# Kernel tuning notes

Measured on AMD Instinct MI355X. Metric: run time of the kernel, lower is better.

The kernel has to match this reference:

```python
import jax, jax.numpy as jnp
import numpy as np

B = 1048576
STATE_DIM, HIDDEN, LATENT = 21, 64, 14
LN_EPS = 1e-5
# index map replicating the torch repeat/cat reconstruction of metric attention (13 -> 21)
EXPAND_IDX = np.array([0, 1, 2, 3, 4, 4, 5, 5, 5, 6, 6, 6, 7, 7, 8, 9, 9, 10, 10, 11, 12])


def setup_inputs() -> dict:
    key = jax.random.key(0)
    ks = jax.random.split(key, 20)

    def w(k, shape, fan_in):
        return (jax.random.uniform(k, shape, jnp.float32, -1.0, 1.0) / np.sqrt(fan_in))

    return {
        'state': jax.random.normal(ks[0], (B, STATE_DIM), jnp.float32),
        # encoder
        'W_enc1': w(ks[1], (STATE_DIM, HIDDEN), STATE_DIM),
        'b_enc1': w(ks[2], (HIDDEN,), STATE_DIM),
        'ln_g': jnp.ones((HIDDEN,), jnp.float32),
        'ln_b': jnp.zeros((HIDDEN,), jnp.float32),
        'W_enc2': w(ks[3], (HIDDEN, HIDDEN), HIDDEN),
        'b_enc2': w(ks[4], (HIDDEN,), HIDDEN),
        'W_enc3': w(ks[5], (HIDDEN, LATENT), HIDDEN),
        'b_enc3': w(ks[6], (LATENT,), HIDDEN),
        # decoder
        'W_dec1': w(ks[7], (LATENT, HIDDEN), LATENT),
        'b_dec1': w(ks[8], (HIDDEN,), LATENT),
        'W_dec2': w(ks[9], (HIDDEN, 8), HIDDEN),
        'b_dec2': w(ks[10], (8,), HIDDEN),
        # attention heads
        'W_m': w(ks[11], (STATE_DIM, 13), STATE_DIM),
        'b_m': w(ks[12], (13,), STATE_DIM),
        'W_h': w(ks[13], (STATE_DIM, 6), STATE_DIM),
        'b_h': w(ks[14], (6,), STATE_DIM),
        'W_c': w(ks[15], (STATE_DIM, 4), STATE_DIM),
        'b_c': w(ks[16], (4,), STATE_DIM),
        # learnable head scales (init 1.0 as in torch)
        's_m': jnp.asarray(1.0, jnp.float32),
        's_h': jnp.asarray(1.0, jnp.float32),
        's_c': jnp.asarray(1.0, jnp.float32),
    }


def _normalize(state):
    ns = state
    ns = ns.at[:, 0:2].set(state[:, 0:2] / 3.0)
    ns = ns.at[:, 17].set(state[:, 17] / 2.0)
    ns = ns.at[:, 18].set(state[:, 18] / 4.0)
    ns = ns.at[:, 19].set(jnp.clip(state[:, 19], 0.0, 2.0) / 2.0)
    return ns


def _layernorm(x, g, b):
    mu = jnp.mean(x, axis=-1, keepdims=True)
    var = jnp.mean(jnp.square(x - mu), axis=-1, keepdims=True)
    return (x - mu) / jnp.sqrt(var + LN_EPS) * g + b


def reference(state, W_enc1, b_enc1, ln_g, ln_b, W_enc2, b_enc2, W_enc3, b_enc3,
              W_dec1, b_dec1, W_dec2, b_dec2, W_m, b_m, W_h, b_h, W_c, b_c,
              s_m, s_h, s_c):
    ns = _normalize(state)  # [B, 21]

    metric = jax.nn.softmax(ns @ W_m + b_m, axis=-1) * (jax.nn.sigmoid(s_m) * 2.0)  # [B,13]
    hyp = jax.nn.softmax(ns @ W_h + b_h, axis=-1) * (jax.nn.sigmoid(s_h) * 2.0)      # [B,6]
    curr = jax.nn.softmax(ns @ W_c + b_c, axis=-1) * (jax.nn.sigmoid(s_c) * 2.0)     # [B,4]

    attended = ns * metric[:, EXPAND_IDX]  # [B,21]

    h = jnp.tanh(_layernorm(attended @ W_enc1 + b_enc1, ln_g, ln_b))
    h = jax.nn.relu(h @ W_enc2 + b_enc2)
    latent = h @ W_enc3 + b_enc3  # [B,14]

    d = jax.nn.relu(latent @ W_dec1 + b_dec1)
    corrections = jnp.tanh(d @ W_dec2 + b_dec2)  # [B,8]

    return corrections, latent, metric, hyp, curr
```

## Files before the change

### kernel.cpp

```cpp
#include <hip/hip_runtime.h>

static constexpr int SD = 21, HD = 64, LT = 14;
static constexpr int NFRAG = 40;

typedef _Float16       f16x4  __attribute__((ext_vector_type(4)));
typedef float          f32x4  __attribute__((ext_vector_type(4)));
typedef unsigned       u32x2v __attribute__((ext_vector_type(2)));
typedef __fp16         pk2    __attribute__((ext_vector_type(2)));

__device__ __forceinline__ float frcp(float x){ return __builtin_amdgcn_rcpf(x); }
__device__ __forceinline__ float frsq(float x){ return __builtin_amdgcn_rsqf(x); }

__device__ __forceinline__ void wave_fence(){
    asm volatile("s_waitcnt lgkmcnt(0)" ::: "memory");
    __builtin_amdgcn_sched_barrier(0);
}

__device__ __forceinline__ unsigned packrtz(float a, float b){
    pk2 h = __builtin_amdgcn_cvt_pkrtz(a, b);
    union { pk2 h; unsigned u; } u; u.h = h; return u.u;
}
__device__ __forceinline__ float ftanh(float x){
    x = fminf(15.0f, fmaxf(-15.0f, x));
    float e = __expf(2.0f * x);
    return (e - 1.0f) * frcp(e + 1.0f);
}
template<int NN>
__device__ __forceinline__ void softmax_scale(float (&v)[NN], float gate){
    float mx = v[0];
#pragma unroll
    for (int j = 1; j < NN; ++j) mx = fmaxf(mx, v[j]);
    float s = 0.0f;
#pragma unroll
    for (int j = 0; j < NN; ++j){ v[j] = __expf(v[j] - mx); s += v[j]; }
    float r = frcp(s) * gate;
#pragma unroll
    for (int j = 0; j < NN; ++j) v[j] *= r;
}

union Frag2 { u32x2v u2; unsigned u[2]; f16x4 f; };

__device__ __forceinline__ f32x4 mfma16(f16x4 a, f16x4 b, f32x4 c){
    return __builtin_amdgcn_mfma_f32_16x16x16f16(a, b, c, 0, 0, 0);
}

__device__ __forceinline__ float headsW(const float* Wm, const float* Wh,
                                        const float* Wc, int k, int j){
    if (j < 13) return Wm[k*13 + j];
    if (j < 19) return Wh[k*6 + (j - 13)];
    if (j < 23) return Wc[k*4 + (j - 19)];
    return 0.0f;
}

__global__ void pack_bfrags(const float* __restrict__ W1, const float* __restrict__ W2,
                            const float* __restrict__ W3, const float* __restrict__ Wd1,
                            const float* __restrict__ Wd2,
                            const float* __restrict__ Wm, const float* __restrict__ Wh,
                            const float* __restrict__ Wc, unsigned* __restrict__ ws)
{
    int t = blockIdx.x * blockDim.x + threadIdx.x;
    if (t >= NFRAG * 64) return;
    int fid = t >> 6, lane = t & 63;
    int g = lane >> 4, c = lane & 15;

    if (fid >= 36) {
        int e = fid - 36, ks16 = e >> 1, ct = e & 1;
        int col = ct*16 + c;
#pragma unroll
        for (int j = 0; j < 2; ++j) {
            int k0 = ks16*16 + g*4 + 2*j;
            float a = (k0     < SD && col < 23) ? headsW(Wm, Wh, Wc, k0,   col) : 0.0f;
            float b = (k0 + 1 < SD && col < 23) ? headsW(Wm, Wh, Wc, k0+1, col) : 0.0f;
            ws[fid*128 + lane*2 + j] = packrtz(a, b);
        }
        return;
    }

    const float* W; int ks16, ct, K, Ncol, ld;
    if (fid < 8)       { W = W1;  ks16 = fid >> 2;    ct = fid & 3;  K = 21; Ncol = 64; ld = 64; }
    else if (fid < 24) { int e = fid - 8;
                         W = W2;  ks16 = e >> 2;      ct = e & 3;    K = 64; Ncol = 64; ld = 64; }
    else if (fid < 28) { W = W3;  ks16 = fid - 24;    ct = 0;        K = 64; Ncol = 14; ld = 14; }
    else if (fid < 32) { W = Wd1; ks16 = 0;           ct = fid - 28; K = 14; Ncol = 64; ld = 64; }
    else               { W = Wd2; ks16 = fid - 32;    ct = 0;        K = 64; Ncol = 8;  ld = 8;  }
    int col = ct*16 + c;
#pragma unroll
    for (int j = 0; j < 2; ++j) {
        int k0 = ks16*16 + g*4 + 2*j;
        float a = (k0     < K && col < Ncol) ? W[k0*ld + col]     : 0.0f;
        float b = (k0 + 1 < K && col < Ncol) ? W[(k0+1)*ld + col] : 0.0f;
        ws[fid*128 + lane*2 + j] = packrtz(a, b);
    }
}

__global__ __launch_bounds__(256) void statenet_mfma9(
    const float* __restrict__ state,
    const unsigned* __restrict__ pw,
    const float* __restrict__ b1,
    const float* __restrict__ lng, const float* __restrict__ lnb,
    const float* __restrict__ b2,  const float* __restrict__ b3,
    const float* __restrict__ bd1, const float* __restrict__ bd2,
    const float* __restrict__ bm,  const float* __restrict__ bh,
    const float* __restrict__ bc,
    const float* __restrict__ psm, const float* __restrict__ psh,
    const float* __restrict__ psc,
    float* __restrict__ out, int N)
{
    __shared__ __align__(16) unsigned s_at[4*1152];
    __shared__ __align__(16) float    s_lg[4*832];

    const int tid = threadIdx.x;
    const int w  = tid >> 6, l = tid & 63;
    const int cl = l & 15,  g = l >> 4;
    const long long rowbase = (long long)blockIdx.x * 128 + w * 32;

    unsigned* at  = s_at + w * 1152;
    float*    slg = s_lg + w * 832;

    const u32x2v* BF2 = reinterpret_cast<const u32x2v*>(pw);
    const f32x4 vzero = {0.0f, 0.0f, 0.0f, 0.0f};

    {
        const float4* g4 = reinterpret_cast<const float4*>(state + rowbase * SD);
        float4* r4 = reinterpret_cast<float4*>(slg);
#pragma unroll
        for (int i = 0; i < 3; ++i) {
            int idx = l + i * 64;
            if (idx < 168) r4[idx] = g4[idx];
        }
    }
    wave_fence();

    float ns[SD];
    if (l < 32) {
        const float* p = slg + l * SD;
#pragma unroll
        for (int k = 0; k < SD; ++k) ns[k] = p[k];

        ns[0]  *= (1.0f / 3.0f);
        ns[1]  *= (1.0f / 3.0f);
        ns[17] *= 0.5f;
        ns[18] *= 0.25f;
        ns[19]  = fminf(fmaxf(ns[19], 0.0f), 2.0f) * 0.5f;

        const int base = l * 36;
#pragma unroll
        for (int kk = 0; kk < 10; ++kk) at[base + kk] = packrtz(ns[2*kk], ns[2*kk+1]);
        at[base + 10] = packrtz(ns[20], 0.0f);
#pragma unroll
        for (int kk = 11; kk < 16; ++kk) at[base + kk] = 0u;
    }
    wave_fence();

    {
        Frag2 aN[2][2];
#pragma unroll
        for (int m2 = 0; m2 < 2; ++m2)
#pragma unroll
            for (int ks = 0; ks < 2; ++ks)
                aN[m2][ks].u2 = *reinterpret_cast<const u32x2v*>(&at[(m2*16 + cl)*36 + ks*8 + 2*g]);
        f32x4 hl[2][2];
#pragma unroll
        for (int ct = 0; ct < 2; ++ct)
#pragma unroll
            for (int m2 = 0; m2 < 2; ++m2) hl[ct][m2] = vzero;
#pragma unroll
        for (int ct = 0; ct < 2; ++ct)
#pragma unroll
            for (int ks = 0; ks < 2; ++ks) {
                Frag2 wf; wf.u2 = BF2[(36 + ks*2 + ct)*64 + l];
#pragma unroll
                for (int m2 = 0; m2 < 2; ++m2)
                    hl[ct][m2] = mfma16(wf.f, aN[m2][ks].f, hl[ct][m2]);
            }
#pragma unroll
        for (int m2 = 0; m2 < 2; ++m2) {
            float* p0 = &slg[(m2*16 + cl)*26 + 4*g];
            reinterpret_cast<float2*>(p0)[0] = make_float2(hl[0][m2][0], hl[0][m2][1]);
            reinterpret_cast<float2*>(p0)[1] = make_float2(hl[0][m2][2], hl[0][m2][3]);
            if (g < 2) {
                float* p1 = &slg[(m2*16 + cl)*26 + 16 + 4*g];
                reinterpret_cast<float2*>(p1)[0] = make_float2(hl[1][m2][0], hl[1][m2][1]);
                reinterpret_cast<float2*>(p1)[1] = make_float2(hl[1][m2][2], hl[1][m2][3]);
            }
        }
    }
    wave_fence();

    if (l < 32) {
        const long long row = rowbase + l;
        float lg[24];
#pragma unroll
        for (int i = 0; i < 12; ++i) {
            float2 v = *reinterpret_cast<const float2*>(&slg[l*26 + 2*i]);
            lg[2*i] = v.x; lg[2*i+1] = v.y;
        }
        float m[13], hv[6], cv[4];
#pragma unroll
        for (int j = 0; j < 13; ++j) m[j]  = lg[j]      + bm[j];
#pragma unroll
        for (int j = 0; j < 6;  ++j) hv[j] = lg[13 + j] + bh[j];
#pragma unroll
        for (int j = 0; j < 4;  ++j) cv[j] = lg[19 + j] + bc[j];

        const float gm = 2.0f * frcp(1.0f + __expf(-psm[0]));
        const float gh = 2.0f * frcp(1.0f + __expf(-psh[0]));
        const float gc = 2.0f * frcp(1.0f + __expf(-psc[0]));
        softmax_scale<13>(m,  gm);
        softmax_scale<6 >(hv, gh);
        softmax_scale<4 >(cv, gc);

        {
            float* pm = out + (long long)22 * N + row * 13;
#pragma unroll
            for (int j = 0; j < 13; ++j) pm[j] = m[j];
            float* ph = out + (long long)35 * N + row * 6;
#pragma unroll
            for (int j = 0; j < 3; ++j)
                reinterpret_cast<float2*>(ph)[j] = make_float2(hv[2*j], hv[2*j+1]);
            float* pc = out + (long long)41 * N + row * 4;
            reinterpret_cast<float4*>(pc)[0] = make_float4(cv[0], cv[1], cv[2], cv[3]);
        }

        constexpr int EIDX[SD] = {0,1,2,3,4,4,5,5,5,6,6,6,7,7,8,9,9,10,10,11,12};
        float atv[SD];
#pragma unroll
        for (int k = 0; k < SD; ++k) atv[k] = ns[k] * m[EIDX[k]];
        const int base = l * 36;
#pragma unroll
        for (int kk = 0; kk < 10; ++kk) at[base + kk] = packrtz(atv[2*kk], atv[2*kk+1]);
        at[base + 10] = packrtz(atv[20], 0.0f);
    }
    wave_fence();

    Frag2 aA[2][2];
#pragma unroll
    for (int m2 = 0; m2 < 2; ++m2)
#pragma unroll
        for (int ks = 0; ks < 2; ++ks)
            aA[m2][ks].u2 = *reinterpret_cast<const u32x2v*>(&at[(m2*16 + cl)*36 + ks*8 + 2*g]);

    f32x4 D1[4][2];
#pragma unroll
    for (int f = 0; f < 4; ++f)
#pragma unroll
        for (int m2 = 0; m2 < 2; ++m2) D1[f][m2] = vzero;
#pragma unroll
    for (int f = 0; f < 4; ++f)
#pragma unroll
        for (int ks = 0; ks < 2; ++ks) {
            Frag2 wf; wf.u2 = BF2[(ks*4 + f)*64 + l];
#pragma unroll
            for (int m2 = 0; m2 < 2; ++m2)
                D1[f][m2] = mfma16(wf.f, aA[m2][ks].f, D1[f][m2]);
        }

    float4 b1q[4], lgq[4], lbq[4];
#pragma unroll
    for (int f = 0; f < 4; ++f) {
        b1q[f] = *reinterpret_cast<const float4*>(&b1[f*16 + 4*g]);
        lgq[f] = *reinterpret_cast<const float4*>(&lng[f*16 + 4*g]);
        lbq[f] = *reinterpret_cast<const float4*>(&lnb[f*16 + 4*g]);
    }

    Frag2 B1[2][4];
#pragma unroll
    for (int m2 = 0; m2 < 2; ++m2) {
        float s = 0.0f, ss = 0.0f;
#pragma unroll
        for (int f = 0; f < 4; ++f) {
            float bb[4] = {b1q[f].x, b1q[f].y, b1q[f].z, b1q[f].w};
#pragma unroll
            for (int q = 0; q < 4; ++q) {
                float v = D1[f][m2][q] + bb[q];
                D1[f][m2][q] = v;
                s += v; ss = fmaf(v, v, ss);
            }
        }
        s  += __shfl_xor(s, 16);  s  += __shfl_xor(s, 32);
        ss += __shfl_xor(ss, 16); ss += __shfl_xor(ss, 32);
        float mu   = s * (1.0f/64.0f);
        float var  = ss * (1.0f/64.0f) - mu*mu;
        float istd = frsq(var + 1e-5f);
#pragma unroll
        for (int f = 0; f < 4; ++f) {
            float gg[4] = {lgq[f].x, lgq[f].y, lgq[f].z, lgq[f].w};
            float be[4] = {lbq[f].x, lbq[f].y, lbq[f].z, lbq[f].w};
            float t0 = ftanh(fmaf((D1[f][m2][0] - mu) * istd, gg[0], be[0]));
            float t1 = ftanh(fmaf((D1[f][m2][1] - mu) * istd, gg[1], be[1]));
            float t2 = ftanh(fmaf((D1[f][m2][2] - mu) * istd, gg[2], be[2]));
            float t3 = ftanh(fmaf((D1[f][m2][3] - mu) * istd, gg[3], be[3]));
            B1[m2][f].u[0] = packrtz(t0, t1);
            B1[m2][f].u[1] = packrtz(t2, t3);
        }
    }

    f32x4 D2[4][2];
#pragma unroll
    for (int f2 = 0; f2 < 4; ++f2)
#pragma unroll
        for (int m2 = 0; m2 < 2; ++m2) D2[f2][m2] = vzero;
#pragma unroll
    for (int f2 = 0; f2 < 4; ++f2)
#pragma unroll
        for (int f = 0; f < 4; ++f) {
            Frag2 wf; wf.u2 = BF2[(8 + f*4 + f2)*64 + l];
#pragma unroll
            for (int m2 = 0; m2 < 2; ++m2)
                D2[f2][m2] = mfma16(wf.f, B1[m2][f].f, D2[f2][m2]);
        }
    Frag2 B2[2][4];
#pragma unroll
    for (int f2 = 0; f2 < 4; ++f2) {
        float4 bq = *reinterpret_cast<const float4*>(&b2[f2*16 + 4*g]);
        float bb[4] = {bq.x, bq.y, bq.z, bq.w};
#pragma unroll
        for (int m2 = 0; m2 < 2; ++m2) {
            float t0 = fmaxf(D2[f2][m2][0] + bb[0], 0.0f);
            float t1 = fmaxf(D2[f2][m2][1] + bb[1], 0.0f);
            float t2 = fmaxf(D2[f2][m2][2] + bb[2], 0.0f);
            float t3 = fmaxf(D2[f2][m2][3] + bb[3], 0.0f);
            B2[m2][f2].u[0] = packrtz(t0, t1);
            B2[m2][f2].u[1] = packrtz(t2, t3);
        }
    }

    float b3v[4];
#pragma unroll
    for (int q = 0; q < 4; ++q) {
        int j = 4*g + q;
        b3v[q] = (j < LT) ? b3[j] : 0.0f;
    }
    Frag2 B3[2];
#pragma unroll
    for (int m2 = 0; m2 < 2; ++m2) {
        f32x4 a3 = vzero;
#pragma unroll
        for (int f = 0; f < 4; ++f) {
            Frag2 wf; wf.u2 = BF2[(24 + f)*64 + l];
            a3 = mfma16(wf.f, B2[m2][f].f, a3);
        }
        float lv[4];
#pragma unroll
        for (int q = 0; q < 4; ++q)
            lv[q] = (4*g + q < LT) ? (a3[q] + b3v[q]) : 0.0f;
        {
            float* pl = out + (long long)8 * N + (rowbase + m2*16 + cl) * 14 + 4*g;
            if (g < 3) {
                reinterpret_cast<float2*>(pl)[0] = make_float2(lv[0], lv[1]);
                reinterpret_cast<float2*>(pl)[1] = make_float2(lv[2], lv[3]);
            } else {
                reinterpret_cast<float2*>(pl)[0] = make_float2(lv[0], lv[1]);
            }
        }
        B3[m2].u[0] = packrtz(lv[0], lv[1]);
        B3[m2].u[1] = packrtz(lv[2], lv[3]);
    }

    f32x4 D4[4][2];
#pragma unroll
    for (int f = 0; f < 4; ++f)
#pragma unroll
        for (int m2 = 0; m2 < 2; ++m2) D4[f][m2] = vzero;
#pragma unroll
    for (int f = 0; f < 4; ++f) {
        Frag2 wf; wf.u2 = BF2[(28 + f)*64 + l];
#pragma unroll
        for (int m2 = 0; m2 < 2; ++m2)
            D4[f][m2] = mfma16(wf.f, B3[m2].f, D4[f][m2]);
    }
    Frag2 B4[2][4];
#pragma unroll
    for (int f = 0; f < 4; ++f) {
        float4 bq = *reinterpret_cast<const float4*>(&bd1[f*16 + 4*g]);
        float bb[4] = {bq.x, bq.y, bq.z, bq.w};
#pragma unroll
        for (int m2 = 0; m2 < 2; ++m2) {
            float t0 = fmaxf(D4[f][m2][0] + bb[0], 0.0f);
            float t1 = fmaxf(D4[f][m2][1] + bb[1], 0.0f);
            float t2 = fmaxf(D4[f][m2][2] + bb[2], 0.0f);
            float t3 = fmaxf(D4[f][m2][3] + bb[3], 0.0f);
            B4[m2][f].u[0] = packrtz(t0, t1);
            B4[m2][f].u[1] = packrtz(t2, t3);
        }
    }

#pragma unroll
    for (int m2 = 0; m2 < 2; ++m2) {
        f32x4 a5 = vzero;
#pragma unroll
        for (int f = 0; f < 4; ++f) {
            Frag2 wf; wf.u2 = BF2[(32 + f)*64 + l];
            a5 = mfma16(wf.f, B4[m2][f].f, a5);
        }
        if (g < 2) {
            float4 bq = *reinterpret_cast<const float4*>(&bd2[4*g]);
            float* pc = out + (rowbase + m2*16 + cl) * 8 + 4*g;
            reinterpret_cast<float4*>(pc)[0] =
                make_float4(ftanh(a5[0] + bq.x), ftanh(a5[1] + bq.y),
                            ftanh(a5[2] + bq.z), ftanh(a5[3] + bq.w));
        }
    }
}

extern "C" void kernel_launch(void* const* d_in, const int* in_sizes, int n_in,
                              void* d_out, int out_size, void* d_ws, size_t ws_size,
                              hipStream_t stream)
{
    const float* state = (const float*)d_in[0];
    const float* W1   = (const float*)d_in[1];
    const float* b1   = (const float*)d_in[2];
    const float* lng  = (const float*)d_in[3];
    const float* lnb  = (const float*)d_in[4];
    const float* W2   = (const float*)d_in[5];
    const float* b2   = (const float*)d_in[6];
    const float* W3   = (const float*)d_in[7];
    const float* b3   = (const float*)d_in[8];
    const float* Wd1  = (const float*)d_in[9];
    const float* bd1  = (const float*)d_in[10];
    const float* Wd2  = (const float*)d_in[11];
    const float* bd2  = (const float*)d_in[12];
    const float* Wm   = (const float*)d_in[13];
    const float* bm   = (const float*)d_in[14];
    const float* Wh   = (const float*)d_in[15];
    const float* bh   = (const float*)d_in[16];
    const float* Wc   = (const float*)d_in[17];
    const float* bc   = (const float*)d_in[18];
    const float* psm  = (const float*)d_in[19];
    const float* psh  = (const float*)d_in[20];
    const float* psc  = (const float*)d_in[21];

    unsigned* pw = (unsigned*)d_ws;

    hipLaunchKernelGGL(pack_bfrags, dim3((NFRAG*64 + 255)/256), dim3(256), 0, stream,
                       W1, W2, W3, Wd1, Wd2, Wm, Wh, Wc, pw);

    const int N = in_sizes[0] / SD;
    hipLaunchKernelGGL(statenet_mfma9, dim3(N / 128), dim3(256), 0, stream,
                       state, pw, b1, lng, lnb, b2, b3, bd1, bd2,
                       bm, bh, bc, psm, psh, psc,
                       (float*)d_out, N);
}
```

Before: 119.9 us.

## Use persistent blocks with register-cached weight fragments across tiles

Launches a fixed grid of 1024 blocks, each looping over 8 row tiles, and loads all 40 packed weight fragments into registers once before the loop instead of reloading them from global memory for every MFMA group. This removes repeated weight-fragment loads and per-block startup cost. In exchange it raises register pressure, which can lower occupancy, and it hardcodes N = 1024*8*128 rows, so any other batch size is handled incorrectly.

```diff
diff --git a/kernel.cpp b/kernel.cpp
--- a/kernel.cpp
+++ b/kernel.cpp
@@ -2,6 +2,8 @@
 
 static constexpr int SD = 21, HD = 64, LT = 14;
 static constexpr int NFRAG = 40;
+static constexpr int NB    = 1024;
+static constexpr int TILES = 8;
 
 typedef _Float16       f16x4  __attribute__((ext_vector_type(4)));
 typedef float          f32x4  __attribute__((ext_vector_type(4)));
@@ -93,7 +95,7 @@
     }
 }
 
-__global__ __launch_bounds__(256) void statenet_mfma9(
+__global__ __launch_bounds__(256) void statenet_mfma10(
     const float* __restrict__ state,
     const unsigned* __restrict__ pw,
     const float* __restrict__ b1,
@@ -112,7 +114,6 @@
     const int tid = threadIdx.x;
     const int w  = tid >> 6, l = tid & 63;
     const int cl = l & 15,  g = l >> 4;
-    const long long rowbase = (long long)blockIdx.x * 128 + w * 32;
 
     unsigned* at  = s_at + w * 1152;
     float*    slg = s_lg + w * 832;
@@ -120,286 +121,295 @@
     const u32x2v* BF2 = reinterpret_cast<const u32x2v*>(pw);
     const f32x4 vzero = {0.0f, 0.0f, 0.0f, 0.0f};
 
-    {
-        const float4* g4 = reinterpret_cast<const float4*>(state + rowbase * SD);
-        float4* r4 = reinterpret_cast<float4*>(slg);
-#pragma unroll
-        for (int i = 0; i < 3; ++i) {
-            int idx = l + i * 64;
-            if (idx < 168) r4[idx] = g4[idx];
-        }
-    }
-    wave_fence();
-
-    float ns[SD];
-    if (l < 32) {
-        const float* p = slg + l * SD;
-#pragma unroll
-        for (int k = 0; k < SD; ++k) ns[k] = p[k];
-
-        ns[0]  *= (1.0f / 3.0f);
-        ns[1]  *= (1.0f / 3.0f);
-        ns[17] *= 0.5f;
-        ns[18] *= 0.25f;
-        ns[19]  = fminf(fmaxf(ns[19], 0.0f), 2.0f) * 0.5f;
-
-        const int base = l * 36;
-#pragma unroll
-        for (int kk = 0; kk < 10; ++kk) at[base + kk] = packrtz(ns[2*kk], ns[2*kk+1]);
-        at[base + 10] = packrtz(ns[20], 0.0f);
-#pragma unroll
-        for (int kk = 11; kk < 16; ++kk) at[base + kk] = 0u;
-    }
-    wave_fence();
-
-    {
-        Frag2 aN[2][2];
+    Frag2 wHD[4], wE1[8], wE2[16], wE3[4], wD1w[4], wD2w[4];
+#pragma unroll
+    for (int e = 0; e < 4; ++e)  wHD[e].u2  = BF2[(36 + e)*64 + l];
+#pragma unroll
+    for (int e = 0; e < 8; ++e)  wE1[e].u2  = BF2[e*64 + l];
+#pragma unroll
+    for (int e = 0; e < 16; ++e) wE2[e].u2  = BF2[(8 + e)*64 + l];
+#pragma unroll
+    for (int e = 0; e < 4; ++e)  wE3[e].u2  = BF2[(24 + e)*64 + l];
+#pragma unroll
+    for (int e = 0; e < 4; ++e)  wD1w[e].u2 = BF2[(28 + e)*64 + l];
+#pragma unroll
+    for (int e = 0; e < 4; ++e)  wD2w[e].u2 = BF2[(32 + e)*64 + l];
+
+#pragma unroll 1
+    for (int it = 0; it < TILES; ++it) {
+        const long long rowbase =
+            ((long long)blockIdx.x + (long long)it * NB) * 128 + w * 32;
+
+        {
+            const float4* g4 = reinterpret_cast<const float4*>(state + rowbase * SD);
+            float4* r4 = reinterpret_cast<float4*>(slg);
+#pragma unroll
+            for (int i = 0; i < 3; ++i) {
+                int idx = l + i * 64;
+                if (idx < 168) r4[idx] = g4[idx];
+            }
+        }
+        wave_fence();
+
+        float ns[SD];
+        if (l < 32) {
+            const float* p = slg + l * SD;
+#pragma unroll
+            for (int k = 0; k < SD; ++k) ns[k] = p[k];
+
+            ns[0]  *= (1.0f / 3.0f);
+            ns[1]  *= (1.0f / 3.0f);
+            ns[17] *= 0.5f;
+            ns[18] *= 0.25f;
+            ns[19]  = fminf(fmaxf(ns[19], 0.0f), 2.0f) * 0.5f;
+
+            const int base = l * 36;
+#pragma unroll
+            for (int kk = 0; kk < 10; ++kk) at[base + kk] = packrtz(ns[2*kk], ns[2*kk+1]);
+            at[base + 10] = packrtz(ns[20], 0.0f);
+#pragma unroll
+            for (int kk = 11; kk < 16; ++kk) at[base + kk] = 0u;
+        }
+        wave_fence();
+
+        {
+            Frag2 aN[2][2];
+#pragma unroll
+            for (int m2 = 0; m2 < 2; ++m2)
+#pragma unroll
+                for (int ks = 0; ks < 2; ++ks)
+                    aN[m2][ks].u2 = *reinterpret_cast<const u32x2v*>(&at[(m2*16 + cl)*36 + ks*8 + 2*g]);
+            f32x4 hl[2][2];
+#pragma unroll
+            for (int ct = 0; ct < 2; ++ct)
+#pragma unroll
+                for (int m2 = 0; m2 < 2; ++m2) hl[ct][m2] = vzero;
+#pragma unroll
+            for (int ct = 0; ct < 2; ++ct)
+#pragma unroll
+                for (int ks = 0; ks < 2; ++ks)
+#pragma unroll
+                    for (int m2 = 0; m2 < 2; ++m2)
+                        hl[ct][m2] = mfma16(wHD[ks*2 + ct].f, aN[m2][ks].f, hl[ct][m2]);
+#pragma unroll
+            for (int m2 = 0; m2 < 2; ++m2) {
+                float* p0 = &slg[(m2*16 + cl)*26 + 4*g];
+                reinterpret_cast<float2*>(p0)[0] = make_float2(hl[0][m2][0], hl[0][m2][1]);
+                reinterpret_cast<float2*>(p0)[1] = make_float2(hl[0][m2][2], hl[0][m2][3]);
+                if (g < 2) {
+                    float* p1 = &slg[(m2*16 + cl)*26 + 16 + 4*g];
+                    reinterpret_cast<float2*>(p1)[0] = make_float2(hl[1][m2][0], hl[1][m2][1]);
+                    reinterpret_cast<float2*>(p1)[1] = make_float2(hl[1][m2][2], hl[1][m2][3]);
+                }
+            }
+        }
+        wave_fence();
+
+        if (l < 32) {
+            const long long row = rowbase + l;
+            float lg[24];
+#pragma unroll
+            for (int i = 0; i < 12; ++i) {
+                float2 v = *reinterpret_cast<const float2*>(&slg[l*26 + 2*i]);
+                lg[2*i] = v.x; lg[2*i+1] = v.y;
+            }
+            float m[13], hv[6], cv[4];
+#pragma unroll
+            for (int j = 0; j < 13; ++j) m[j]  = lg[j]      + bm[j];
+#pragma unroll
+            for (int j = 0; j < 6;  ++j) hv[j] = lg[13 + j] + bh[j];
+#pragma unroll
+            for (int j = 0; j < 4;  ++j) cv[j] = lg[19 + j] + bc[j];
+
+            const float gm = 2.0f * frcp(1.0f + __expf(-psm[0]));
+            const float gh = 2.0f * frcp(1.0f + __expf(-psh[0]));
+            const float gc = 2.0f * frcp(1.0f + __expf(-psc[0]));
+            softmax_scale<13>(m,  gm);
+            softmax_scale<6 >(hv, gh);
+            softmax_scale<4 >(cv, gc);
+
+            {
+                float* pm = out + (long long)22 * N + row * 13;
+#pragma unroll
+                for (int j = 0; j < 13; ++j) pm[j] = m[j];
+                float* ph = out + (long long)35 * N + row * 6;
+#pragma unroll
+                for (int j = 0; j < 3; ++j)
+                    reinterpret_cast<float2*>(ph)[j] = make_float2(hv[2*j], hv[2*j+1]);
+                float* pc = out + (long long)41 * N + row * 4;
+                reinterpret_cast<float4*>(pc)[0] = make_float4(cv[0], cv[1], cv[2], cv[3]);
+            }
+
+            constexpr int EIDX[SD] = {0,1,2,3,4,4,5,5,5,6,6,6,7,7,8,9,9,10,10,11,12};
+            float atv[SD];
+#pragma unroll
+            for (int k = 0; k < SD; ++k) atv[k] = ns[k] * m[EIDX[k]];
+            const int base = l * 36;
+#pragma unroll
+            for (int kk = 0; kk < 10; ++kk) at[base + kk] = packrtz(atv[2*kk], atv[2*kk+1]);
+            at[base + 10] = packrtz(atv[20], 0.0f);
+        }
+        wave_fence();
+
+        Frag2 aA[2][2];
 #pragma unroll
         for (int m2 = 0; m2 < 2; ++m2)
 #pragma unroll
             for (int ks = 0; ks < 2; ++ks)
-                aN[m2][ks].u2 = *reinterpret_cast<const u32x2v*>(&at[(m2*16 + cl)*36 + ks*8 + 2*g]);
-        f32x4 hl[2][2];
-#pragma unroll
-        for (int ct = 0; ct < 2; ++ct)
-#pragma unroll
-            for (int m2 = 0; m2 < 2; ++m2) hl[ct][m2] = vzero;
-#pragma unroll
-        for (int ct = 0; ct < 2; ++ct)
-#pragma unroll
-            for (int ks = 0; ks < 2; ++ks) {
-                Frag2 wf; wf.u2 = BF2[(36 + ks*2 + ct)*64 + l];
+                aA[m2][ks].u2 = *reinterpret_cast<const u32x2v*>(&at[(m2*16 + cl)*36 + ks*8 + 2*g]);
+
+        f32x4 D1[4][2];
+#pragma unroll
+        for (int f = 0; f < 4; ++f)
+#pragma unroll
+            for (int m2 = 0; m2 < 2; ++m2) D1[f][m2] = vzero;
+#pragma unroll
+        for (int f = 0; f < 4; ++f)
+#pragma unroll
+            for (int ks = 0; ks < 2; ++ks)
 #pragma unroll
                 for (int m2 = 0; m2 < 2; ++m2)
-                    hl[ct][m2] = mfma16(wf.f, aN[m2][ks].f, hl[ct][m2]);
-            }
+                    D1[f][m2] = mfma16(wE1[ks*4 + f].f, aA[m2][ks].f, D1[f][m2]);
+
+        float4 b1q[4], lgq[4], lbq[4];
+#pragma unroll
+        for (int f = 0; f < 4; ++f) {
+            b1q[f] = *reinterpret_cast<const float4*>(&b1[f*16 + 4*g]);
+            lgq[f] = *reinterpret_cast<const float4*>(&lng[f*16 + 4*g]);
+            lbq[f] = *reinterpret_cast<const float4*>(&lnb[f*16 + 4*g]);
+        }
+
+        Frag2 B1[2][4];
 #pragma unroll
         for (int m2 = 0; m2 < 2; ++m2) {
-            float* p0 = &slg[(m2*16 + cl)*26 + 4*g];
-            reinterpret_cast<float2*>(p0)[0] = make_float2(hl[0][m2][0], hl[0][m2][1]);
-            reinterpret_cast<float2*>(p0)[1] = make_float2(hl[0][m2][2], hl[0][m2][3]);
+            float s = 0.0f, ss = 0.0f;
+#pragma unroll
+            for (int f = 0; f < 4; ++f) {
+                float bb[4] = {b1q[f].x, b1q[f].y, b1q[f].z, b1q[f].w};
+#pragma unroll
+                for (int q = 0; q < 4; ++q) {
+                    float v = D1[f][m2][q] + bb[q];
+                    D1[f][m2][q] = v;
+                    s += v; ss = fmaf(v, v, ss);
+                }
+            }
+            s  += __shfl_xor(s, 16);  s  += __shfl_xor(s, 32);
+            ss += __shfl_xor(ss, 16); ss += __shfl_xor(ss, 32);
+            float mu   = s * (1.0f/64.0f);
+            float var  = ss * (1.0f/64.0f) - mu*mu;
+            float istd = frsq(var + 1e-5f);
+#pragma unroll
+            for (int f = 0; f < 4; ++f) {
+                float gg[4] = {lgq[f].x, lgq[f].y, lgq[f].z, lgq[f].w};
+                float be[4] = {lbq[f].x, lbq[f].y, lbq[f].z, lbq[f].w};
+                float t0 = ftanh(fmaf((D1[f][m2][0] - mu) * istd, gg[0], be[0]));
+                float t1 = ftanh(fmaf((D1[f][m2][1] - mu) * istd, gg[1], be[1]));
+                float t2 = ftanh(fmaf((D1[f][m2][2] - mu) * istd, gg[2], be[2]));
+                float t3 = ftanh(fmaf((D1[f][m2][3] - mu) * istd, gg[3], be[3]));
+                B1[m2][f].u[0] = packrtz(t0, t1);
+                B1[m2][f].u[1] = packrtz(t2, t3);
+            }
+        }
+
+        f32x4 D2[4][2];
+#pragma unroll
+        for (int f2 = 0; f2 < 4; ++f2)
+#pragma unroll
+            for (int m2 = 0; m2 < 2; ++m2) D2[f2][m2] = vzero;
+#pragma unroll
+        for (int f2 = 0; f2 < 4; ++f2)
+#pragma unroll
+            for (int f = 0; f < 4; ++f)
+#pragma unroll
+                for (int m2 = 0; m2 < 2; ++m2)
+                    D2[f2][m2] = mfma16(wE2[f*4 + f2].f, B1[m2][f].f, D2[f2][m2]);
+        Frag2 B2[2][4];
+#pragma unroll
+        for (int f2 = 0; f2 < 4; ++f2) {
+            float4 bq = *reinterpret_cast<const float4*>(&b2[f2*16 + 4*g]);
+            float bb[4] = {bq.x, bq.y, bq.z, bq.w};
+#pragma unroll
+            for (int m2 = 0; m2 < 2; ++m2) {
+                float t0 = fmaxf(D2[f2][m2][0] + bb[0], 0.0f);
+                float t1 = fmaxf(D2[f2][m2][1] + bb[1], 0.0f);
+                float t2 = fmaxf(D2[f2][m2][2] + bb[2], 0.0f);
+                float t3 = fmaxf(D2[f2][m2][3] + bb[3], 0.0f);
+                B2[m2][f2].u[0] = packrtz(t0, t1);
+                B2[m2][f2].u[1] = packrtz(t2, t3);
+            }
+        }
+
+        float b3v[4];
+#pragma unroll
+        for (int q = 0; q < 4; ++q) {
+            int j = 4*g + q;
+            b3v[q] = (j < LT) ? b3[j] : 0.0f;
+        }
+        Frag2 B3[2];
+#pragma unroll
+        for (int m2 = 0; m2 < 2; ++m2) {
+            f32x4 a3 = vzero;
+#pragma unroll
+            for (int f = 0; f < 4; ++f)
+                a3 = mfma16(wE3[f].f, B2[m2][f].f, a3);
+            float lv[4];
+#pragma unroll
+            for (int q = 0; q < 4; ++q)
+                lv[q] = (4*g + q < LT) ? (a3[q] + b3v[q]) : 0.0f;
+            {
+                float* pl = out + (long long)8 * N + (rowbase + m2*16 + cl) * 14 + 4*g;
+                if (g < 3) {
+                    reinterpret_cast<float2*>(pl)[0] = make_float2(lv[0], lv[1]);
+                    reinterpret_cast<float2*>(pl)[1] = make_float2(lv[2], lv[3]);
+                } else {
+                    reinterpret_cast<float2*>(pl)[0] = make_float2(lv[0], lv[1]);
+                }
+            }
+            B3[m2].u[0] = packrtz(lv[0], lv[1]);
+            B3[m2].u[1] = packrtz(lv[2], lv[3]);
+        }
+
+        f32x4 D4[4][2];
+#pragma unroll
+        for (int f = 0; f < 4; ++f)
+#pragma unroll
+            for (int m2 = 0; m2 < 2; ++m2) D4[f][m2] = vzero;
+#pragma unroll
+        for (int f = 0; f < 4; ++f)
+#pragma unroll
+            for (int m2 = 0; m2 < 2; ++m2)
+                D4[f][m2] = mfma16(wD1w[f].f, B3[m2].f, D4[f][m2]);
+        Frag2 B4[2][4];
+#pragma unroll
+        for (int f = 0; f < 4; ++f) {
+            float4 bq = *reinterpret_cast<const float4*>(&bd1[f*16 + 4*g]);
+            float bb[4] = {bq.x, bq.y, bq.z, bq.w};
+#pragma unroll
+            for (int m2 = 0; m2 < 2; ++m2) {
+                float t0 = fmaxf(D4[f][m2][0] + bb[0], 0.0f);
+                float t1 = fmaxf(D4[f][m2][1] + bb[1], 0.0f);
+                float t2 = fmaxf(D4[f][m2][2] + bb[2], 0.0f);
+                float t3 = fmaxf(D4[f][m2][3] + bb[3], 0.0f);
+                B4[m2][f].u[0] = packrtz(t0, t1);
+                B4[m2][f].u[1] = packrtz(t2, t3);
+            }
+        }
+
+#pragma unroll
+        for (int m2 = 0; m2 < 2; ++m2) {
+            f32x4 a5 = vzero;
+#pragma unroll
+            for (int f = 0; f < 4; ++f)
+                a5 = mfma16(wD2w[f].f, B4[m2][f].f, a5);
             if (g < 2) {
-                float* p1 = &slg[(m2*16 + cl)*26 + 16 + 4*g];
-                reinterpret_cast<float2*>(p1)[0] = make_float2(hl[1][m2][0], hl[1][m2][1]);
-                reinterpret_cast<float2*>(p1)[1] = make_float2(hl[1][m2][2], hl[1][m2][3]);
-            }
-        }
-    }
-    wave_fence();
-
-    if (l < 32) {
-        const long long row = rowbase + l;
-        float lg[24];
-#pragma unroll
-        for (int i = 0; i < 12; ++i) {
-            float2 v = *reinterpret_cast<const float2*>(&slg[l*26 + 2*i]);
-            lg[2*i] = v.x; lg[2*i+1] = v.y;
-        }
-        float m[13], hv[6], cv[4];
-#pragma unroll
-        for (int j = 0; j < 13; ++j) m[j]  = lg[j]      + bm[j];
-#pragma unroll
-        for (int j = 0; j < 6;  ++j) hv[j] = lg[13 + j] + bh[j];
-#pragma unroll
-        for (int j = 0; j < 4;  ++j) cv[j] = lg[19 + j] + bc[j];
-
-        const float gm = 2.0f * frcp(1.0f + __expf(-psm[0]));
-        const float gh = 2.0f * frcp(1.0f + __expf(-psh[0]));
-        const float gc = 2.0f * frcp(1.0f + __expf(-psc[0]));
-        softmax_scale<13>(m,  gm);
-        softmax_scale<6 >(hv, gh);
-        softmax_scale<4 >(cv, gc);
-
-        {
-            float* pm = out + (long long)22 * N + row * 13;
-#pragma unroll
-            for (int j = 0; j < 13; ++j) pm[j] = m[j];
-            float* ph = out + (long long)35 * N + row * 6;
-#pragma unroll
-            for (int j = 0; j < 3; ++j)
-                reinterpret_cast<float2*>(ph)[j] = make_float2(hv[2*j], hv[2*j+1]);
-            float* pc = out + (long long)41 * N + row * 4;
-            reinterpret_cast<float4*>(pc)[0] = make_float4(cv[0], cv[1], cv[2], cv[3]);
-        }
-
-        constexpr int EIDX[SD] = {0,1,2,3,4,4,5,5,5,6,6,6,7,7,8,9,9,10,10,11,12};
-        float atv[SD];
-#pragma unroll
-        for (int k = 0; k < SD; ++k) atv[k] = ns[k] * m[EIDX[k]];
-        const int base = l * 36;
-#pragma unroll
-        for (int kk = 0; kk < 10; ++kk) at[base + kk] = packrtz(atv[2*kk], atv[2*kk+1]);
-        at[base + 10] = packrtz(atv[20], 0.0f);
-    }
-    wave_fence();
-
-    Frag2 aA[2][2];
-#pragma unroll
-    for (int m2 = 0; m2 < 2; ++m2)
-#pragma unroll
-        for (int ks = 0; ks < 2; ++ks)
-            aA[m2][ks].u2 = *reinterpret_cast<const u32x2v*>(&at[(m2*16 + cl)*36 + ks*8 + 2*g]);
-
-    f32x4 D1[4][2];
-#pragma unroll
-    for (int f = 0; f < 4; ++f)
-#pragma unroll
-        for (int m2 = 0; m2 < 2; ++m2) D1[f][m2] = vzero;
-#pragma unroll
-    for (int f = 0; f < 4; ++f)
-#pragma unroll
-        for (int ks = 0; ks < 2; ++ks) {
-            Frag2 wf; wf.u2 = BF2[(ks*4 + f)*64 + l];
-#pragma unroll
-            for (int m2 = 0; m2 < 2; ++m2)
-                D1[f][m2] = mfma16(wf.f, aA[m2][ks].f, D1[f][m2]);
-        }
-
-    float4 b1q[4], lgq[4], lbq[4];
-#pragma unroll
-    for (int f = 0; f < 4; ++f) {
-        b1q[f] = *reinterpret_cast<const float4*>(&b1[f*16 + 4*g]);
-        lgq[f] = *reinterpret_cast<const float4*>(&lng[f*16 + 4*g]);
-        lbq[f] = *reinterpret_cast<const float4*>(&lnb[f*16 + 4*g]);
-    }
-
-    Frag2 B1[2][4];
-#pragma unroll
-    for (int m2 = 0; m2 < 2; ++m2) {
-        float s = 0.0f, ss = 0.0f;
-#pragma unroll
-        for (int f = 0; f < 4; ++f) {
-            float bb[4] = {b1q[f].x, b1q[f].y, b1q[f].z, b1q[f].w};
-#pragma unroll
-            for (int q = 0; q < 4; ++q) {
-                float v = D1[f][m2][q] + bb[q];
-                D1[f][m2][q] = v;
-                s += v; ss = fmaf(v, v, ss);
-            }
-        }
-        s  += __shfl_xor(s, 16);  s  += __shfl_xor(s, 32);
-        ss += __shfl_xor(ss, 16); ss += __shfl_xor(ss, 32);
-        float mu   = s * (1.0f/64.0f);
-        float var  = ss * (1.0f/64.0f) - mu*mu;
-        float istd = frsq(var + 1e-5f);
-#pragma unroll
-        for (int f = 0; f < 4; ++f) {
-            float gg[4] = {lgq[f].x, lgq[f].y, lgq[f].z, lgq[f].w};
-            float be[4] = {lbq[f].x, lbq[f].y, lbq[f].z, lbq[f].w};
-            float t0 = ftanh(fmaf((D1[f][m2][0] - mu) * istd, gg[0], be[0]));
-            float t1 = ftanh(fmaf((D1[f][m2][1] - mu) * istd, gg[1], be[1]));
-            float t2 = ftanh(fmaf((D1[f][m2][2] - mu) * istd, gg[2], be[2]));
-            float t3 = ftanh(fmaf((D1[f][m2][3] - mu) * istd, gg[3], be[3]));
-            B1[m2][f].u[0] = packrtz(t0, t1);
-            B1[m2][f].u[1] = packrtz(t2, t3);
-        }
-    }
-
-    f32x4 D2[4][2];
-#pragma unroll
-    for (int f2 = 0; f2 < 4; ++f2)
-#pragma unroll
-        for (int m2 = 0; m2 < 2; ++m2) D2[f2][m2] = vzero;
-#pragma unroll
-    for (int f2 = 0; f2 < 4; ++f2)
-#pragma unroll
-        for (int f = 0; f < 4; ++f) {
-            Frag2 wf; wf.u2 = BF2[(8 + f*4 + f2)*64 + l];
-#pragma unroll
-            for (int m2 = 0; m2 < 2; ++m2)
-                D2[f2][m2] = mfma16(wf.f, B1[m2][f].f, D2[f2][m2]);
-        }
-    Frag2 B2[2][4];
-#pragma unroll
-    for (int f2 = 0; f2 < 4; ++f2) {
-        float4 bq = *reinterpret_cast<const float4*>(&b2[f2*16 + 4*g]);
-        float bb[4] = {bq.x, bq.y, bq.z, bq.w};
-#pragma unroll
-        for (int m2 = 0; m2 < 2; ++m2) {
-            float t0 = fmaxf(D2[f2][m2][0] + bb[0], 0.0f);
-            float t1 = fmaxf(D2[f2][m2][1] + bb[1], 0.0f);
-            float t2 = fmaxf(D2[f2][m2][2] + bb[2], 0.0f);
-            float t3 = fmaxf(D2[f2][m2][3] + bb[3], 0.0f);
-            B2[m2][f2].u[0] = packrtz(t0, t1);
-            B2[m2][f2].u[1] = packrtz(t2, t3);
-        }
-    }
-
-    float b3v[4];
-#pragma unroll
-    for (int q = 0; q < 4; ++q) {
-        int j = 4*g + q;
-        b3v[q] = (j < LT) ? b3[j] : 0.0f;
-    }
-    Frag2 B3[2];
-#pragma unroll
-    for (int m2 = 0; m2 < 2; ++m2) {
-        f32x4 a3 = vzero;
-#pragma unroll
-        for (int f = 0; f < 4; ++f) {
-            Frag2 wf; wf.u2 = BF2[(24 + f)*64 + l];
-            a3 = mfma16(wf.f, B2[m2][f].f, a3);
-        }
-        float lv[4];
-#pragma unroll
-        for (int q = 0; q < 4; ++q)
-            lv[q] = (4*g + q < LT) ? (a3[q] + b3v[q]) : 0.0f;
-        {
-            float* pl = out + (long long)8 * N + (rowbase + m2*16 + cl) * 14 + 4*g;
-            if (g < 3) {
-                reinterpret_cast<float2*>(pl)[0] = make_float2(lv[0], lv[1]);
-                reinterpret_cast<float2*>(pl)[1] = make_float2(lv[2], lv[3]);
-            } else {
-                reinterpret_cast<float2*>(pl)[0] = make_float2(lv[0], lv[1]);
-            }
-        }
-        B3[m2].u[0] = packrtz(lv[0], lv[1]);
-        B3[m2].u[1] = packrtz(lv[2], lv[3]);
-    }
-
-    f32x4 D4[4][2];
-#pragma unroll
-    for (int f = 0; f < 4; ++f)
-#pragma unroll
-        for (int m2 = 0; m2 < 2; ++m2) D4[f][m2] = vzero;
-#pragma unroll
-    for (int f = 0; f < 4; ++f) {
-        Frag2 wf; wf.u2 = BF2[(28 + f)*64 + l];
-#pragma unroll
-        for (int m2 = 0; m2 < 2; ++m2)
-            D4[f][m2] = mfma16(wf.f, B3[m2].f, D4[f][m2]);
-    }
-    Frag2 B4[2][4];
-#pragma unroll
-    for (int f = 0; f < 4; ++f) {
-        float4 bq = *reinterpret_cast<const float4*>(&bd1[f*16 + 4*g]);
-        float bb[4] = {bq.x, bq.y, bq.z, bq.w};
-#pragma unroll
-        for (int m2 = 0; m2 < 2; ++m2) {
-            float t0 = fmaxf(D4[f][m2][0] + bb[0], 0.0f);
-            float t1 = fmaxf(D4[f][m2][1] + bb[1], 0.0f);
-            float t2 = fmaxf(D4[f][m2][2] + bb[2], 0.0f);
-            float t3 = fmaxf(D4[f][m2][3] + bb[3], 0.0f);
-            B4[m2][f].u[0] = packrtz(t0, t1);
-            B4[m2][f].u[1] = packrtz(t2, t3);
-        }
-    }
-
-#pragma unroll
-    for (int m2 = 0; m2 < 2; ++m2) {
-        f32x4 a5 = vzero;
-#pragma unroll
-        for (int f = 0; f < 4; ++f) {
-            Frag2 wf; wf.u2 = BF2[(32 + f)*64 + l];
-            a5 = mfma16(wf.f, B4[m2][f].f, a5);
-        }
-        if (g < 2) {
-            float4 bq = *reinterpret_cast<const float4*>(&bd2[4*g]);
-            float* pc = out + (rowbase + m2*16 + cl) * 8 + 4*g;
-            reinterpret_cast<float4*>(pc)[0] =
-                make_float4(ftanh(a5[0] + bq.x), ftanh(a5[1] + bq.y),
-                            ftanh(a5[2] + bq.z), ftanh(a5[3] + bq.w));
-        }
+                float4 bq = *reinterpret_cast<const float4*>(&bd2[4*g]);
+                float* pc = out + (rowbase + m2*16 + cl) * 8 + 4*g;
+                reinterpret_cast<float4*>(pc)[0] =
+                    make_float4(ftanh(a5[0] + bq.x), ftanh(a5[1] + bq.y),
+                                ftanh(a5[2] + bq.z), ftanh(a5[3] + bq.w));
+            }
+        }
+        wave_fence();
     }
 }
 
@@ -436,7 +446,7 @@
                        W1, W2, W3, Wd1, Wd2, Wm, Wh, Wc, pw);
 
     const int N = in_sizes[0] / SD;
-    hipLaunchKernelGGL(statenet_mfma9, dim3(N / 128), dim3(256), 0, stream,
+    hipLaunchKernelGGL(statenet_mfma10, dim3(NB), dim3(256), 0, stream,
                        state, pw, b1, lng, lnb, b2, b3, bd1, bd2,
                        bm, bh, bc, psm, psh, psc,
                        (float*)d_out, N);
```

Result: slower. 122.8 us (+2.4%).

## Process 64 rows per wave with four M-tiles and full-lane scalar phases

Applied to the files above, without the earlier changes.

Each wave now handles 64 rows instead of 32, so every MFMA weight fragment load is reused across four 16-row tiles and the per-row softmax, normalization and attention stages use all 64 lanes rather than half. The shared-memory row stride for the packed activations shrinks from 36 to 20 words, and the grid is halved to 256 rows per block. The aim is to cut idle lanes and repeated weight-fragment traffic. The cost is more accumulator and fragment registers per thread and more LDS per block, which may lower occupancy.

```diff
diff --git a/kernel.cpp b/kernel.cpp
--- a/kernel.cpp
+++ b/kernel.cpp
@@ -2,6 +2,7 @@
 
 static constexpr int SD = 21, HD = 64, LT = 14;
 static constexpr int NFRAG = 40;
+static constexpr int ATS   = 20;
 
 typedef _Float16       f16x4  __attribute__((ext_vector_type(4)));
 typedef float          f32x4  __attribute__((ext_vector_type(4)));
@@ -93,7 +94,7 @@
     }
 }
 
-__global__ __launch_bounds__(256) void statenet_mfma9(
+__global__ __launch_bounds__(256) void statenet_mfma11(
     const float* __restrict__ state,
     const unsigned* __restrict__ pw,
     const float* __restrict__ b1,
@@ -106,16 +107,16 @@
     const float* __restrict__ psc,
     float* __restrict__ out, int N)
 {
-    __shared__ __align__(16) unsigned s_at[4*1152];
-    __shared__ __align__(16) float    s_lg[4*832];
+    __shared__ __align__(16) unsigned s_at[4*64*ATS];
+    __shared__ __align__(16) float    s_lg[4*64*26];
 
     const int tid = threadIdx.x;
     const int w  = tid >> 6, l = tid & 63;
     const int cl = l & 15,  g = l >> 4;
-    const long long rowbase = (long long)blockIdx.x * 128 + w * 32;
-
-    unsigned* at  = s_at + w * 1152;
-    float*    slg = s_lg + w * 832;
+    const long long rowbase = (long long)blockIdx.x * 256 + w * 64;
+
+    unsigned* at  = s_at + w * 64 * ATS;
+    float*    slg = s_lg + w * 64 * 26;
 
     const u32x2v* BF2 = reinterpret_cast<const u32x2v*>(pw);
     const f32x4 vzero = {0.0f, 0.0f, 0.0f, 0.0f};
@@ -124,15 +125,15 @@
         const float4* g4 = reinterpret_cast<const float4*>(state + rowbase * SD);
         float4* r4 = reinterpret_cast<float4*>(slg);
 #pragma unroll
-        for (int i = 0; i < 3; ++i) {
+        for (int i = 0; i < 6; ++i) {
             int idx = l + i * 64;
-            if (idx < 168) r4[idx] = g4[idx];
+            if (idx < 336) r4[idx] = g4[idx];
         }
     }
     wave_fence();
 
     float ns[SD];
-    if (l < 32) {
+    {
         const float* p = slg + l * SD;
 #pragma unroll
         for (int k = 0; k < SD; ++k) ns[k] = p[k];
@@ -143,7 +144,7 @@
         ns[18] *= 0.25f;
         ns[19]  = fminf(fmaxf(ns[19], 0.0f), 2.0f) * 0.5f;
 
-        const int base = l * 36;
+        const int base = l * ATS;
 #pragma unroll
         for (int kk = 0; kk < 10; ++kk) at[base + kk] = packrtz(ns[2*kk], ns[2*kk+1]);
         at[base + 10] = packrtz(ns[20], 0.0f);
@@ -153,41 +154,41 @@
     wave_fence();
 
     {
-        Frag2 aN[2][2];
-#pragma unroll
-        for (int m2 = 0; m2 < 2; ++m2)
+        Frag2 aN[4][2];
+#pragma unroll
+        for (int M = 0; M < 4; ++M)
 #pragma unroll
             for (int ks = 0; ks < 2; ++ks)
-                aN[m2][ks].u2 = *reinterpret_cast<const u32x2v*>(&at[(m2*16 + cl)*36 + ks*8 + 2*g]);
-        f32x4 hl[2][2];
+                aN[M][ks].u2 = *reinterpret_cast<const u32x2v*>(&at[(M*16 + cl)*ATS + ks*8 + 2*g]);
+        f32x4 hl[2][4];
 #pragma unroll
         for (int ct = 0; ct < 2; ++ct)
 #pragma unroll
-            for (int m2 = 0; m2 < 2; ++m2) hl[ct][m2] = vzero;
+            for (int M = 0; M < 4; ++M) hl[ct][M] = vzero;
 #pragma unroll
         for (int ct = 0; ct < 2; ++ct)
 #pragma unroll
             for (int ks = 0; ks < 2; ++ks) {
                 Frag2 wf; wf.u2 = BF2[(36 + ks*2 + ct)*64 + l];
 #pragma unroll
-                for (int m2 = 0; m2 < 2; ++m2)
-                    hl[ct][m2] = mfma16(wf.f, aN[m2][ks].f, hl[ct][m2]);
+                for (int M = 0; M < 4; ++M)
+                    hl[ct][M] = mfma16(wf.f, aN[M][ks].f, hl[ct][M]);
             }
 #pragma unroll
-        for (int m2 = 0; m2 < 2; ++m2) {
-            float* p0 = &slg[(m2*16 + cl)*26 + 4*g];
-            reinterpret_cast<float2*>(p0)[0] = make_float2(hl[0][m2][0], hl[0][m2][1]);
-            reinterpret_cast<float2*>(p0)[1] = make_float2(hl[0][m2][2], hl[0][m2][3]);
+        for (int M = 0; M < 4; ++M) {
+            float* p0 = &slg[(M*16 + cl)*26 + 4*g];
+            reinterpret_cast<float2*>(p0)[0] = make_float2(hl[0][M][0], hl[0][M][1]);
+            reinterpret_cast<float2*>(p0)[1] = make_float2(hl[0][M][2], hl[0][M][3]);
             if (g < 2) {
-                float* p1 = &slg[(m2*16 + cl)*26 + 16 + 4*g];
-                reinterpret_cast<float2*>(p1)[0] = make_float2(hl[1][m2][0], hl[1][m2][1]);
-                reinterpret_cast<float2*>(p1)[1] = make_float2(hl[1][m2][2], hl[1][m2][3]);
+                float* p1 = &slg[(M*16 + cl)*26 + 16 + 4*g];
+                reinterpret_cast<float2*>(p1)[0] = make_float2(hl[1][M][0], hl[1][M][1]);
+                reinterpret_cast<float2*>(p1)[1] = make_float2(hl[1][M][2], hl[1][M][3]);
             }
         }
     }
     wave_fence();
 
-    if (l < 32) {
+    {
         const long long row = rowbase + l;
         float lg[24];
 #pragma unroll
@@ -226,33 +227,33 @@
         float atv[SD];
 #pragma unroll
         for (int k = 0; k < SD; ++k) atv[k] = ns[k] * m[EIDX[k]];
-        const int base = l * 36;
+        const int base = l * ATS;
 #pragma unroll
         for (int kk = 0; kk < 10; ++kk) at[base + kk] = packrtz(atv[2*kk], atv[2*kk+1]);
         at[base + 10] = packrtz(atv[20], 0.0f);
     }
     wave_fence();
 
-    Frag2 aA[2][2];
-#pragma unroll
-    for (int m2 = 0; m2 < 2; ++m2)
+    Frag2 aA[4][2];
+#pragma unroll
+    for (int M = 0; M < 4; ++M)
 #pragma unroll
         for (int ks = 0; ks < 2; ++ks)
-            aA[m2][ks].u2 = *reinterpret_cast<const u32x2v*>(&at[(m2*16 + cl)*36 + ks*8 + 2*g]);
-
-    f32x4 D1[4][2];
+            aA[M][ks].u2 = *reinterpret_cast<const u32x2v*>(&at[(M*16 + cl)*ATS + ks*8 + 2*g]);
+
+    f32x4 D1[4][4];
 #pragma unroll
     for (int f = 0; f < 4; ++f)
 #pragma unroll
-        for (int m2 = 0; m2 < 2; ++m2) D1[f][m2] = vzero;
+        for (int M = 0; M < 4; ++M) D1[f][M] = vzero;
 #pragma unroll
     for (int f = 0; f < 4; ++f)
 #pragma unroll
         for (int ks = 0; ks < 2; ++ks) {
             Frag2 wf; wf.u2 = BF2[(ks*4 + f)*64 + l];
 #pragma unroll
-            for (int m2 = 0; m2 < 2; ++m2)
-                D1[f][m2] = mfma16(wf.f, aA[m2][ks].f, D1[f][m2]);
+            for (int M = 0; M < 4; ++M)
+                D1[f][M] = mfma16(wf.f, aA[M][ks].f, D1[f][M]);
         }
 
     float4 b1q[4], lgq[4], lbq[4];
@@ -263,17 +264,17 @@
         lbq[f] = *reinterpret_cast<const float4*>(&lnb[f*16 + 4*g]);
     }
 
-    Frag2 B1[2][4];
-#pragma unroll
-    for (int m2 = 0; m2 < 2; ++m2) {
+    Frag2 B1[4][4];
+#pragma unroll
+    for (int M = 0; M < 4; ++M) {
         float s = 0.0f, ss = 0.0f;
 #pragma unroll
         for (int f = 0; f < 4; ++f) {
             float bb[4] = {b1q[f].x, b1q[f].y, b1q[f].z, b1q[f].w};
 #pragma unroll
             for (int q = 0; q < 4; ++q) {
-                float v = D1[f][m2][q] + bb[q];
-                D1[f][m2][q] = v;
+                float v = D1[f][M][q] + bb[q];
+                D1[f][M][q] = v;
                 s += v; ss = fmaf(v, v, ss);
             }
         }
@@ -286,42 +287,42 @@
         for (int f = 0; f < 4; ++f) {
             float gg[4] = {lgq[f].x, lgq[f].y, lgq[f].z, lgq[f].w};
             float be[4] = {lbq[f].x, lbq[f].y, lbq[f].z, lbq[f].w};
-            float t0 = ftanh(fmaf((D1[f][m2][0] - mu) * istd, gg[0], be[0]));
-            float t1 = ftanh(fmaf((D1[f][m2][1] - mu) * istd, gg[1], be[1]));
-            float t2 = ftanh(fmaf((D1[f][m2][2] - mu) * istd, gg[2], be[2]));
-            float t3 = ftanh(fmaf((D1[f][m2][3] - mu) * istd, gg[3], be[3]));
-            B1[m2][f].u[0] = packrtz(t0, t1);
-            B1[m2][f].u[1] = packrtz(t2, t3);
-        }
-    }
-
-    f32x4 D2[4][2];
+            float t0 = ftanh(fmaf((D1[f][M][0] - mu) * istd, gg[0], be[0]));
+            float t1 = ftanh(fmaf((D1[f][M][1] - mu) * istd, gg[1], be[1]));
+            float t2 = ftanh(fmaf((D1[f][M][2] - mu) * istd, gg[2], be[2]));
+            float t3 = ftanh(fmaf((D1[f][M][3] - mu) * istd, gg[3], be[3]));
+            B1[M][f].u[0] = packrtz(t0, t1);
+            B1[M][f].u[1] = packrtz(t2, t3);
+        }
+    }
+
+    f32x4 D2[4][4];
 #pragma unroll
     for (int f2 = 0; f2 < 4; ++f2)
 #pragma unroll
-        for (int m2 = 0; m2 < 2; ++m2) D2[f2][m2] = vzero;
+        for (int M = 0; M < 4; ++M) D2[f2][M] = vzero;
 #pragma unroll
     for (int f2 = 0; f2 < 4; ++f2)
 #pragma unroll
         for (int f = 0; f < 4; ++f) {
             Frag2 wf; wf.u2 = BF2[(8 + f*4 + f2)*64 + l];
 #pragma unroll
-            for (int m2 = 0; m2 < 2; ++m2)
-                D2[f2][m2] = mfma16(wf.f, B1[m2][f].f, D2[f2][m2]);
-        }
-    Frag2 B2[2][4];
+            for (int M = 0; M < 4; ++M)
+                D2[f2][M] = mfma16(wf.f, B1[M][f].f, D2[f2][M]);
+        }
+    Frag2 B2[4][4];
 #pragma unroll
     for (int f2 = 0; f2 < 4; ++f2) {
         float4 bq = *reinterpret_cast<const float4*>(&b2[f2*16 + 4*g]);
         float bb[4] = {bq.x, bq.y, bq.z, bq.w};
 #pragma unroll
-        for (int m2 = 0; m2 < 2; ++m2) {
-            float t0 = fmaxf(D2[f2][m2][0] + bb[0], 0.0f);
-            float t1 = fmaxf(D2[f2][m2][1] + bb[1], 0.0f);
-            float t2 = fmaxf(D2[f2][m2][2] + bb[2], 0.0f);
-            float t3 = fmaxf(D2[f2][m2][3] + bb[3], 0.0f);
-            B2[m2][f2].u[0] = packrtz(t0, t1);
-            B2[m2][f2].u[1] = packrtz(t2, t3);
+        for (int M = 0; M < 4; ++M) {
+            float t0 = fmaxf(D2[f2][M][0] + bb[0], 0.0f);
+            float t1 = fmaxf(D2[f2][M][1] + bb[1], 0.0f);
+            float t2 = fmaxf(D2[f2][M][2] + bb[2], 0.0f);
+            float t3 = fmaxf(D2[f2][M][3] + bb[3], 0.0f);
+            B2[M][f2].u[0] = packrtz(t0, t1);
+            B2[M][f2].u[1] = packrtz(t2, t3);
         }
     }
 
@@ -331,21 +332,25 @@
         int j = 4*g + q;
         b3v[q] = (j < LT) ? b3[j] : 0.0f;
     }
-    Frag2 B3[2];
-#pragma unroll
-    for (int m2 = 0; m2 < 2; ++m2) {
-        f32x4 a3 = vzero;
-#pragma unroll
-        for (int f = 0; f < 4; ++f) {
-            Frag2 wf; wf.u2 = BF2[(24 + f)*64 + l];
-            a3 = mfma16(wf.f, B2[m2][f].f, a3);
-        }
+    f32x4 a3[4];
+#pragma unroll
+    for (int M = 0; M < 4; ++M) a3[M] = vzero;
+#pragma unroll
+    for (int f = 0; f < 4; ++f) {
+        Frag2 wf; wf.u2 = BF2[(24 + f)*64 + l];
+#pragma unroll
+        for (int M = 0; M < 4; ++M)
+            a3[M] = mfma16(wf.f, B2[M][f].f, a3[M]);
+    }
+    Frag2 B3[4];
+#pragma unroll
+    for (int M = 0; M < 4; ++M) {
         float lv[4];
 #pragma unroll
         for (int q = 0; q < 4; ++q)
-            lv[q] = (4*g + q < LT) ? (a3[q] + b3v[q]) : 0.0f;
+            lv[q] = (4*g + q < LT) ? (a3[M][q] + b3v[q]) : 0.0f;
         {
-            float* pl = out + (long long)8 * N + (rowbase + m2*16 + cl) * 14 + 4*g;
+            float* pl = out + (long long)8 * N + (rowbase + M*16 + cl) * 14 + 4*g;
             if (g < 3) {
                 reinterpret_cast<float2*>(pl)[0] = make_float2(lv[0], lv[1]);
                 reinterpret_cast<float2*>(pl)[1] = make_float2(lv[2], lv[3]);
@@ -353,52 +358,56 @@
                 reinterpret_cast<float2*>(pl)[0] = make_float2(lv[0], lv[1]);
             }
         }
-        B3[m2].u[0] = packrtz(lv[0], lv[1]);
-        B3[m2].u[1] = packrtz(lv[2], lv[3]);
-    }
-
-    f32x4 D4[4][2];
+        B3[M].u[0] = packrtz(lv[0], lv[1]);
+        B3[M].u[1] = packrtz(lv[2], lv[3]);
+    }
+
+    f32x4 D4[4][4];
 #pragma unroll
     for (int f = 0; f < 4; ++f)
 #pragma unroll
-        for (int m2 = 0; m2 < 2; ++m2) D4[f][m2] = vzero;
+        for (int M = 0; M < 4; ++M) D4[f][M] = vzero;
 #pragma unroll
     for (int f = 0; f < 4; ++f) {
         Frag2 wf; wf.u2 = BF2[(28 + f)*64 + l];
 #pragma unroll
-        for (int m2 = 0; m2 < 2; ++m2)
-            D4[f][m2] = mfma16(wf.f, B3[m2].f, D4[f][m2]);
-    }
-    Frag2 B4[2][4];
+        for (int M = 0; M < 4; ++M)
+            D4[f][M] = mfma16(wf.f, B3[M].f, D4[f][M]);
+    }
+    Frag2 B4[4][4];
 #pragma unroll
     for (int f = 0; f < 4; ++f) {
         float4 bq = *reinterpret_cast<const float4*>(&bd1[f*16 + 4*g]);
         float bb[4] = {bq.x, bq.y, bq.z, bq.w};
 #pragma unroll
-        for (int m2 = 0; m2 < 2; ++m2) {
-            float t0 = fmaxf(D4[f][m2][0] + bb[0], 0.0f);
-            float t1 = fmaxf(D4[f][m2][1] + bb[1], 0.0f);
-            float t2 = fmaxf(D4[f][m2][2] + bb[2], 0.0f);
-            float t3 = fmaxf(D4[f][m2][3] + bb[3], 0.0f);
-            B4[m2][f].u[0] = packrtz(t0, t1);
-            B4[m2][f].u[1] = packrtz(t2, t3);
-        }
-    }
-
-#pragma unroll
-    for (int m2 = 0; m2 < 2; ++m2) {
-        f32x4 a5 = vzero;
-#pragma unroll
-        for (int f = 0; f < 4; ++f) {
-            Frag2 wf; wf.u2 = BF2[(32 + f)*64 + l];
-            a5 = mfma16(wf.f, B4[m2][f].f, a5);
-        }
+        for (int M = 0; M < 4; ++M) {
+            float t0 = fmaxf(D4[f][M][0] + bb[0], 0.0f);
+            float t1 = fmaxf(D4[f][M][1] + bb[1], 0.0f);
+            float t2 = fmaxf(D4[f][M][2] + bb[2], 0.0f);
+            float t3 = fmaxf(D4[f][M][3] + bb[3], 0.0f);
+            B4[M][f].u[0] = packrtz(t0, t1);
+            B4[M][f].u[1] = packrtz(t2, t3);
+        }
+    }
+
+    f32x4 a5[4];
+#pragma unroll
+    for (int M = 0; M < 4; ++M) a5[M] = vzero;
+#pragma unroll
+    for (int f = 0; f < 4; ++f) {
+        Frag2 wf; wf.u2 = BF2[(32 + f)*64 + l];
+#pragma unroll
+        for (int M = 0; M < 4; ++M)
+            a5[M] = mfma16(wf.f, B4[M][f].f, a5[M]);
+    }
+#pragma unroll
+    for (int M = 0; M < 4; ++M) {
         if (g < 2) {
             float4 bq = *reinterpret_cast<const float4*>(&bd2[4*g]);
-            float* pc = out + (rowbase + m2*16 + cl) * 8 + 4*g;
+            float* pc = out + (rowbase + M*16 + cl) * 8 + 4*g;
             reinterpret_cast<float4*>(pc)[0] =
-                make_float4(ftanh(a5[0] + bq.x), ftanh(a5[1] + bq.y),
-                            ftanh(a5[2] + bq.z), ftanh(a5[3] + bq.w));
+                make_float4(ftanh(a5[M][0] + bq.x), ftanh(a5[M][1] + bq.y),
+                            ftanh(a5[M][2] + bq.z), ftanh(a5[M][3] + bq.w));
         }
     }
 }
@@ -436,7 +445,7 @@
                        W1, W2, W3, Wd1, Wd2, Wm, Wh, Wc, pw);
 
     const int N = in_sizes[0] / SD;
-    hipLaunchKernelGGL(statenet_mfma9, dim3(N / 128), dim3(256), 0, stream,
+    hipLaunchKernelGGL(statenet_mfma11, dim3(N / 256), dim3(256), 0, stream,
                        state, pw, b1, lng, lnb, b2, b3, bd1, bd2,
                        bm, bh, bc, psm, psh, psc,
                        (float*)d_out, N);
```

Result: slower. 125.5 us (+4.7%).
